# Optimization experiments

Hardware: AMD Instinct MI355X
Metric: run time of the kernel (lower is better)

Reference implementation:

```python
import math
import jax, jax.numpy as jnp
import numpy as np

B, S, D, H, F = 2, 2048, 1024, 16, 4096
HD = D // H
EPS = 1e-6
ALPHA, BETA = 0.5, 1.0  # SpectralActivation defaults


def setup_inputs() -> dict:
    key = jax.random.key(0)
    ks = jax.random.split(key, 24)
    init = lambda k, shape: (jax.random.normal(k, shape, jnp.float32) * 0.02)
    return {
        "x": jax.random.normal(ks[0], (B, S, D), jnp.float32),
        # attention params (W stored as [in, out], i.e. y = x @ W + b)
        "Wq": init(ks[1], (D, D)), "bq": jnp.zeros((D,), jnp.float32),
        "Wk": init(ks[2], (D, D)), "bk": jnp.zeros((D,), jnp.float32),
        "Wv": init(ks[3], (D, D)), "bv": jnp.zeros((D,), jnp.float32),
        "Wo": init(ks[4], (D, D)), "bo": jnp.zeros((D,), jnp.float32),
        "resonance": jnp.ones((H, 1, 1), jnp.float32),
        "phase": jnp.zeros((H, 1, 1), jnp.float32),
        # norm1
        "g1": jnp.ones((D,), jnp.float32), "b1": jnp.zeros((D,), jnp.float32),
        "s1": jnp.full((1,), 0.1, jnp.float32),
        # FFN
        "W1": init(ks[5], (D, F)), "bf1": jnp.zeros((F,), jnp.float32),
        "W2": init(ks[6], (F, D)), "bf2": jnp.zeros((D,), jnp.float32),
        # norm2
        "g2": jnp.ones((D,), jnp.float32), "b2": jnp.zeros((D,), jnp.float32),
        "s2": jnp.full((1,), 0.1, jnp.float32),
    }


def _harmonic_ln(x, gamma, beta, stab):
    mean = jnp.mean(x, axis=-1, keepdims=True)
    std = jnp.std(x, axis=-1, keepdims=True, ddof=1)  # torch std is unbiased
    std = std + stab * jnp.sin(std * math.pi)
    return gamma * ((x - mean) / (std + EPS)) + beta


def _spectral_act(x):
    c = math.sqrt(2.0 / math.pi)
    gelu_like = 0.5 * x * (1.0 + jnp.tanh(c * (x + 0.044715 * x ** 3)))
    return gelu_like + ALPHA * jnp.sin(BETA * x)


def _forward(x, Wq, bq, Wk, bk, Wv, bv, Wo, bo, resonance, phase,
             g1, b1, s1, W1, bf1, W2, bf2, g2, b2, s2):
    Bq, Sq, _ = x.shape
    q = (x @ Wq + bq).reshape(Bq, Sq, H, HD).transpose(0, 2, 1, 3)  # [B,H,S,hd]
    k = (x @ Wk + bk).reshape(Bq, Sq, H, HD).transpose(0, 2, 1, 3)
    v = (x @ Wv + bv).reshape(Bq, Sq, H, HD).transpose(0, 2, 1, 3)

    scores = jnp.einsum('bhqd,bhkd->bhqk', q, k) / math.sqrt(HD)  # [B,H,S,S]
    scores = scores + resonance[None] * jnp.sin(scores + phase[None])
    attn = jax.nn.softmax(scores, axis=-1)
    out = jnp.einsum('bhqk,bhkd->bhqd', attn, v)
    out = out.transpose(0, 2, 1, 3).reshape(Bq, Sq, D)
    attn_out = out @ Wo + bo

    x = _harmonic_ln(x + attn_out, g1, b1, s1)
    ff = _spectral_act(x @ W1 + bf1) @ W2 + bf2
    x = _harmonic_ln(x + ff, g2, b2, s2)
    return x


def reference(x, Wq, bq, Wk, bk, Wv, bv, Wo, bo, resonance, phase,
              g1, b1, s1, W1, bf1, W2, bf2, g2, b2, s2):
    return _forward(x, Wq, bq, Wk, bk, Wv, bv, Wo, bo, resonance, phase,
                    g1, b1, s1, W1, bf1, W2, bf2, g2, b2, s2)
```

## Files before the change

### kernel.cpp

```cpp
#include <hip/hip_runtime.h>
#include <cstdint>
#include <cstddef>


typedef float  f32x4  __attribute__((ext_vector_type(4)));
typedef __bf16 bf16x8 __attribute__((ext_vector_type(8)));
typedef unsigned short u16x8 __attribute__((ext_vector_type(8)));
typedef unsigned short u16x4 __attribute__((ext_vector_type(4)));

#define MFMA_BF16(a, b, c) __builtin_amdgcn_mfma_f32_16x16x32_bf16((a), (b), (c), 0, 0, 0)

static __device__ __forceinline__ unsigned short f32_to_bf16(float f) {
  unsigned int u = __float_as_uint(f);
  u += 0x7fffu + ((u >> 16) & 1u);
  return (unsigned short)(u >> 16);
}
static __device__ __forceinline__ float bf16_to_f32(unsigned short h) {
  return __uint_as_float(((unsigned int)h) << 16);
}
static __device__ __forceinline__ bf16x8 lds_frag(const unsigned short* base, int byte) {
  return __builtin_bit_cast(bf16x8, *(const u16x8*)((const char*)base + byte));
}
static __device__ __forceinline__ float spectral_act(float x) {
  const float c = 0.7978845608028654f;
  float g = 0.5f * x * (1.0f + tanhf(c * (x + 0.044715f * x * x * x)));
  return g + 0.5f * __sinf(x);
}

__global__ __launch_bounds__(256) void cvt_f32_bf16(const float* __restrict__ in,
                                                    unsigned short* __restrict__ out, int n) {
  int i = (blockIdx.x * 256 + threadIdx.x) * 4;
  if (i < n) {
    float4 v = *(const float4*)(in + i);
    u16x4 o;
    o[0] = f32_to_bf16(v.x); o[1] = f32_to_bf16(v.y);
    o[2] = f32_to_bf16(v.z); o[3] = f32_to_bf16(v.w);
    *(u16x4*)(out + i) = o;
  }
}

__global__ __launch_bounds__(256) void transpose_f32_bf16(const float* __restrict__ W,
                                                          unsigned short* __restrict__ Wt,
                                                          int K, int N) {
  __shared__ float tile[32][33];
  int tx = threadIdx.x & 31, ty = threadIdx.x >> 5;
  int k0 = blockIdx.y * 32, n0 = blockIdx.x * 32;
#pragma unroll
  for (int i = 0; i < 4; i++)
    tile[ty + i * 8][tx] = W[(size_t)(k0 + ty + i * 8) * N + n0 + tx];
  __syncthreads();
#pragma unroll
  for (int i = 0; i < 4; i++)
    Wt[(size_t)(n0 + ty + i * 8) * K + k0 + tx] = f32_to_bf16(tile[tx][ty + i * 8]);
}

template <int BM, int BN, int EPI>
__global__ __launch_bounds__(256) void gemm_bt(const unsigned short* __restrict__ A,
                                               const unsigned short* __restrict__ Bt,
                                               const float* __restrict__ bias,
                                               unsigned short* __restrict__ Cb,
                                               float* __restrict__ Cf,
                                               int M, int N, int K) {
  constexpr int MI = BM / 32;
  constexpr int NI = BN / 32;
  __shared__ unsigned short As[BM * 32];
  __shared__ unsigned short Bs[BN * 32];
  const int t = threadIdx.x;
  const int lane = t & 63, w = t >> 6;
  const int wr = w >> 1, wc = w & 1;
  const int g = lane >> 4, cc = lane & 15;
  const int row0 = blockIdx.y * BM, col0 = blockIdx.x * BN;

  f32x4 acc[MI][NI];
#pragma unroll
  for (int mi = 0; mi < MI; mi++)
#pragma unroll
    for (int ni = 0; ni < NI; ni++) acc[mi][ni] = (f32x4){0.f, 0.f, 0.f, 0.f};

  const int nk = K >> 5;
  const int sr = t >> 2, sc = (t & 3) * 8;

  for (int kt = 0; kt < nk; ++kt) {
    __syncthreads();
#pragma unroll
    for (int i = 0; i < BM / 64; ++i) {
      int r = sr + i * 64;
      u16x8 v = *(const u16x8*)(A + (size_t)(row0 + r) * K + (kt << 5) + sc);
      *(u16x8*)((char*)As + ((r * 64 + sc * 2) ^ ((r & 7) << 4))) = v;
    }
#pragma unroll
    for (int i = 0; i < BN / 64; ++i) {
      int r = sr + i * 64;
      u16x8 v = *(const u16x8*)(Bt + (size_t)(col0 + r) * K + (kt << 5) + sc);
      *(u16x8*)((char*)Bs + ((r * 64 + sc * 2) ^ ((r & 7) << 4))) = v;
    }
    __syncthreads();

    bf16x8 af[MI], bg[NI];
#pragma unroll
    for (int mi = 0; mi < MI; mi++) {
      int r = wr * (BM / 2) + mi * 16 + cc;
      af[mi] = lds_frag(As, (r * 64 + g * 16) ^ ((r & 7) << 4));
    }
#pragma unroll
    for (int ni = 0; ni < NI; ni++) {
      int r = wc * (BN / 2) + ni * 16 + cc;
      bg[ni] = lds_frag(Bs, (r * 64 + g * 16) ^ ((r & 7) << 4));
    }
#pragma unroll
    for (int mi = 0; mi < MI; mi++)
#pragma unroll
      for (int ni = 0; ni < NI; ni++)
        acc[mi][ni] = MFMA_BF16(af[mi], bg[ni], acc[mi][ni]);
  }

#pragma unroll
  for (int mi = 0; mi < MI; mi++) {
#pragma unroll
    for (int ni = 0; ni < NI; ni++) {
      int col = col0 + wc * (BN / 2) + ni * 16 + cc;
      float bv = bias[col];
#pragma unroll
      for (int r4 = 0; r4 < 4; r4++) {
        int row = row0 + wr * (BM / 2) + mi * 16 + g * 4 + r4;
        float val = acc[mi][ni][r4] + bv;
        if (EPI == 2) val = spectral_act(val);
        if (EPI == 0 || EPI == 2) Cb[(size_t)row * N + col] = f32_to_bf16(val);
        else                      Cf[(size_t)row * N + col] = val;
      }
    }
  }
}

__global__ __launch_bounds__(256) void attn_fused(const unsigned short* __restrict__ Qb,
                                                  const unsigned short* __restrict__ Kb,
                                                  const unsigned short* __restrict__ Vb,
                                                  int ld,
                                                  const float* __restrict__ resonance,
                                                  const float* __restrict__ phase,
                                                  unsigned short* __restrict__ O, int ldo) {
  constexpr int S = 2048;
  __shared__ unsigned short Ks[64 * 64];
  __shared__ unsigned short Vs[64 * 64];
  __shared__ unsigned short Ps[4][16 * 64];

  const int t = threadIdx.x, lane = t & 63, w = t >> 6;
  const int g = lane >> 4, cc = lane & 15;
  const int bh = blockIdx.y, b = bh >> 4, h = bh & 15;
  const int q0 = blockIdx.x * 64 + w * 16;
  const float res = resonance[h], ph = phase[h];

  const unsigned short* Qh = Qb + (size_t)b * S * ld + h * 64;
  const unsigned short* Kh = Kb + (size_t)b * S * ld + h * 64;
  const unsigned short* Vh = Vb + (size_t)b * S * ld + h * 64;

  bf16x8 qa0, qa1;
  {
    const unsigned short* qp = Qh + (size_t)(q0 + cc) * ld + g * 8;
    qa0 = __builtin_bit_cast(bf16x8, *(const u16x8*)qp);
    qa1 = __builtin_bit_cast(bf16x8, *(const u16x8*)(qp + 32));
  }

  f32x4 oacc[4];
#pragma unroll
  for (int i = 0; i < 4; i++) oacc[i] = (f32x4){0.f, 0.f, 0.f, 0.f};
  float Mx[4] = {-1e30f, -1e30f, -1e30f, -1e30f};
  float Lx[4] = {0.f, 0.f, 0.f, 0.f};
  char* PsW = (char*)&Ps[w][0];

  for (int kt = 0; kt < S / 64; ++kt) {
    __syncthreads();
    {
      int r = t >> 3, c8 = (t & 7) * 8;
      const unsigned short* kp = Kh + (size_t)(kt * 64) * ld;
#pragma unroll
      for (int hh = 0; hh < 2; ++hh) {
        int row = r + hh * 32;
        u16x8 v = *(const u16x8*)(kp + (size_t)row * ld + c8);
        *(u16x8*)((char*)Ks + ((row * 128 + c8 * 2) ^ ((row & 7) << 4))) = v;
      }
      int key = t & 63, hb0 = (t >> 6) * 16;
      const unsigned short* vp = Vh + (size_t)(kt * 64 + key) * ld + hb0;
      u16x8 v0 = *(const u16x8*)vp;
      u16x8 v1 = *(const u16x8*)(vp + 8);
#pragma unroll
      for (int j = 0; j < 8; j++) {
        int hd0 = hb0 + j;
        *(unsigned short*)((char*)Vs + ((hd0 * 128 + key * 2) ^ ((hd0 & 7) << 4))) = v0[j];
        int hd1 = hb0 + 8 + j;
        *(unsigned short*)((char*)Vs + ((hd1 * 128 + key * 2) ^ ((hd1 & 7) << 4))) = v1[j];
      }
    }
    __syncthreads();

    f32x4 sacc[4];
#pragma unroll
    for (int nb = 0; nb < 4; nb++) sacc[nb] = (f32x4){0.f, 0.f, 0.f, 0.f};
#pragma unroll
    for (int nb = 0; nb < 4; nb++) {
      int key = nb * 16 + cc;
      int rb = key * 128, xr = (key & 7) << 4;
      bf16x8 k0 = lds_frag(Ks, (rb + g * 16) ^ xr);
      bf16x8 k1 = lds_frag(Ks, (rb + 64 + g * 16) ^ xr);
      sacc[nb] = MFMA_BF16(qa0, k0, sacc[nb]);
      sacc[nb] = MFMA_BF16(qa1, k1, sacc[nb]);
    }

    float sm[4] = {-1e30f, -1e30f, -1e30f, -1e30f};
#pragma unroll
    for (int nb = 0; nb < 4; nb++)
#pragma unroll
      for (int r4 = 0; r4 < 4; r4++) {
        float sv = sacc[nb][r4] * 0.125f;
        sv += res * __sinf(sv + ph);
        sacc[nb][r4] = sv;
        sm[r4] = fmaxf(sm[r4], sv);
      }
#pragma unroll
    for (int d = 1; d < 16; d <<= 1)
#pragma unroll
      for (int r4 = 0; r4 < 4; r4++) sm[r4] = fmaxf(sm[r4], __shfl_xor(sm[r4], d, 16));

    float alpha[4], psum[4] = {0.f, 0.f, 0.f, 0.f};
#pragma unroll
    for (int r4 = 0; r4 < 4; r4++) {
      float nm = fmaxf(Mx[r4], sm[r4]);
      alpha[r4] = __expf(Mx[r4] - nm);
      Mx[r4] = nm;
    }
#pragma unroll
    for (int nb = 0; nb < 4; nb++)
#pragma unroll
      for (int r4 = 0; r4 < 4; r4++) {
        float p = __expf(sacc[nb][r4] - Mx[r4]);
        unsigned short pu = f32_to_bf16(p);
        psum[r4] += bf16_to_f32(pu);
        int prow = g * 4 + r4, pcol = nb * 16 + cc;
        *(unsigned short*)(PsW + ((prow * 128 + pcol * 2) ^ ((prow & 7) << 4))) = pu;
      }
#pragma unroll
    for (int d = 1; d < 16; d <<= 1)
#pragma unroll
      for (int r4 = 0; r4 < 4; r4++) psum[r4] += __shfl_xor(psum[r4], d, 16);
#pragma unroll
    for (int r4 = 0; r4 < 4; r4++) Lx[r4] = Lx[r4] * alpha[r4] + psum[r4];
#pragma unroll
    for (int nb2 = 0; nb2 < 4; nb2++)
#pragma unroll
      for (int r4 = 0; r4 < 4; r4++) oacc[nb2][r4] *= alpha[r4];

    bf16x8 pa0, pa1;
    {
      int xr = (cc & 7) << 4;
      pa0 = lds_frag((const unsigned short*)PsW, (cc * 128 + g * 16) ^ xr);
      pa1 = lds_frag((const unsigned short*)PsW, (cc * 128 + 64 + g * 16) ^ xr);
    }
#pragma unroll
    for (int nb2 = 0; nb2 < 4; nb2++) {
      int hd = nb2 * 16 + cc;
      int rb = hd * 128, xr = (hd & 7) << 4;
      bf16x8 v0 = lds_frag(Vs, (rb + g * 16) ^ xr);
      bf16x8 v1 = lds_frag(Vs, (rb + 64 + g * 16) ^ xr);
      oacc[nb2] = MFMA_BF16(pa0, v0, oacc[nb2]);
      oacc[nb2] = MFMA_BF16(pa1, v1, oacc[nb2]);
    }
  }

#pragma unroll
  for (int nb2 = 0; nb2 < 4; nb2++)
#pragma unroll
    for (int r4 = 0; r4 < 4; r4++) {
      float ov = oacc[nb2][r4] / Lx[r4];
      O[(size_t)(b * S + q0 + g * 4 + r4) * ldo + h * 64 + nb2 * 16 + cc] = f32_to_bf16(ov);
    }
}

__global__ __launch_bounds__(256) void resid_harmonic_ln(const float* __restrict__ xin,
                                                         const float* __restrict__ radd,
                                                         const float* __restrict__ gamma,
                                                         const float* __restrict__ beta,
                                                         const float* __restrict__ stab,
                                                         float* __restrict__ yf,
                                                         unsigned short* __restrict__ yb) {
  const int row = blockIdx.x, t = threadIdx.x;
  const float* xr = xin + (size_t)row * 1024;
  const float* rr = radd + (size_t)row * 1024;
  float v[4], s = 0.f, ss = 0.f;
#pragma unroll
  for (int j = 0; j < 4; j++) {
    int idx = t + j * 256;
    v[j] = xr[idx] + rr[idx];
    s += v[j]; ss += v[j] * v[j];
  }
#pragma unroll
  for (int d = 1; d < 64; d <<= 1) { s += __shfl_xor(s, d); ss += __shfl_xor(ss, d); }
  __shared__ float sb[8];
  int lane = t & 63, wid = t >> 6;
  if (lane == 0) { sb[wid] = s; sb[4 + wid] = ss; }
  __syncthreads();
  s = sb[0] + sb[1] + sb[2] + sb[3];
  ss = sb[4] + sb[5] + sb[6] + sb[7];
  float mean = s * (1.f / 1024.f);
  float var = fmaxf((ss - 1024.f * mean * mean) * (1.f / 1023.f), 0.f);
  float sd = sqrtf(var);
  sd += stab[0] * sinf(sd * 3.14159265358979323846f);
  float inv = 1.f / (sd + 1e-6f);
#pragma unroll
  for (int j = 0; j < 4; j++) {
    int idx = t + j * 256;
    float y = gamma[idx] * ((v[j] - mean) * inv) + beta[idx];
    yf[(size_t)row * 1024 + idx] = y;
    if (yb) yb[(size_t)row * 1024 + idx] = f32_to_bf16(y);
  }
}

extern "C" void kernel_launch(void* const* d_in, const int* in_sizes, int n_in,
                              void* d_out, int out_size, void* d_ws, size_t ws_size,
                              hipStream_t stream) {
  const float* x    = (const float*)d_in[0];
  const float* Wq   = (const float*)d_in[1];
  const float* bq   = (const float*)d_in[2];
  const float* Wk   = (const float*)d_in[3];
  const float* bk   = (const float*)d_in[4];
  const float* Wv   = (const float*)d_in[5];
  const float* bv   = (const float*)d_in[6];
  const float* Wo   = (const float*)d_in[7];
  const float* bo   = (const float*)d_in[8];
  const float* reso = (const float*)d_in[9];
  const float* phas = (const float*)d_in[10];
  const float* g1   = (const float*)d_in[11];
  const float* b1   = (const float*)d_in[12];
  const float* s1   = (const float*)d_in[13];
  const float* W1   = (const float*)d_in[14];
  const float* bf1  = (const float*)d_in[15];
  const float* W2   = (const float*)d_in[16];
  const float* bf2  = (const float*)d_in[17];
  const float* g2   = (const float*)d_in[18];
  const float* b2   = (const float*)d_in[19];
  const float* s2   = (const float*)d_in[20];

  const int BS = 4096;

  char* ws = (char*)d_ws;
  const size_t OFF_QKV  = 0;
  const size_t OFF_XB   = 25165824;
  const size_t OFF_WQKV = 33554432;
  const size_t OFF_WOT  = 39845888;
  const size_t OFF_W1T  = 41943040;
  const size_t OFF_W2T  = 50331648;
  const size_t OFF_BQKV = 58720256;
  const size_t OFF_T0   = 58736640;
  const size_t OFF_X1   = 75513856;
  const size_t OFF_X1B  = 92291072;

  unsigned short* qkv   = (unsigned short*)(ws + OFF_QKV);
  unsigned short* xb    = (unsigned short*)(ws + OFF_XB);
  unsigned short* ao    = (unsigned short*)(ws + OFF_XB);
  unsigned short* Wqkvt = (unsigned short*)(ws + OFF_WQKV);
  unsigned short* Wot   = (unsigned short*)(ws + OFF_WOT);
  unsigned short* W1t   = (unsigned short*)(ws + OFF_W1T);
  unsigned short* W2t   = (unsigned short*)(ws + OFF_W2T);
  float*          bqkv  = (float*)(ws + OFF_BQKV);
  float*          t0    = (float*)(ws + OFF_T0);
  float*          x1    = (float*)(ws + OFF_X1);
  unsigned short* x1b   = (unsigned short*)(ws + OFF_X1B);
  unsigned short* hb    = (unsigned short*)(ws + OFF_QKV);
  float*          out   = (float*)d_out;

  cvt_f32_bf16<<<4096, 256, 0, stream>>>(x, xb, BS * 1024);

  transpose_f32_bf16<<<dim3(32, 32), 256, 0, stream>>>(Wq, Wqkvt, 1024, 1024);
  transpose_f32_bf16<<<dim3(32, 32), 256, 0, stream>>>(Wk, Wqkvt + (size_t)1024 * 1024, 1024, 1024);
  transpose_f32_bf16<<<dim3(32, 32), 256, 0, stream>>>(Wv, Wqkvt + (size_t)2048 * 1024, 1024, 1024);
  transpose_f32_bf16<<<dim3(32, 32), 256, 0, stream>>>(Wo, Wot, 1024, 1024);
  transpose_f32_bf16<<<dim3(128, 32), 256, 0, stream>>>(W1, W1t, 1024, 4096);
  transpose_f32_bf16<<<dim3(32, 128), 256, 0, stream>>>(W2, W2t, 4096, 1024);

  hipMemcpyAsync((void*)bqkv,          (const void*)bq, 1024 * 4, hipMemcpyDeviceToDevice, stream);
  hipMemcpyAsync((void*)(bqkv + 1024), (const void*)bk, 1024 * 4, hipMemcpyDeviceToDevice, stream);
  hipMemcpyAsync((void*)(bqkv + 2048), (const void*)bv, 1024 * 4, hipMemcpyDeviceToDevice, stream);

  gemm_bt<128, 128, 0><<<dim3(24, 32), 256, 0, stream>>>(xb, Wqkvt, bqkv, qkv, nullptr,
                                                         4096, 3072, 1024);

  attn_fused<<<dim3(32, 32), 256, 0, stream>>>(qkv, qkv + 1024, qkv + 2048, 3072,
                                               reso, phas, ao, 1024);

  gemm_bt<128, 64, 1><<<dim3(16, 32), 256, 0, stream>>>(ao, Wot, bo, nullptr, t0,
                                                        4096, 1024, 1024);

  resid_harmonic_ln<<<4096, 256, 0, stream>>>(x, t0, g1, b1, s1, x1, x1b);

  gemm_bt<128, 128, 2><<<dim3(32, 32), 256, 0, stream>>>(x1b, W1t, bf1, hb, nullptr,
                                                         4096, 4096, 1024);

  gemm_bt<128, 64, 1><<<dim3(16, 32), 256, 0, stream>>>(hb, W2t, bf2, nullptr, t0,
                                                        4096, 1024, 4096);

  resid_harmonic_ln<<<4096, 256, 0, stream>>>(x1, t0, g2, b2, s2, out, nullptr);
}
```

Baseline: 528.9 us.

## Use direct global-to-LDS loads in GEMM and transposed LDS reads for V in attention

The GEMM tile loads now use global_load_lds to write straight into shared memory with a new XOR chunk swizzle, and the barrier moves to the end of each k iteration. In attention, V is stored row-major in per-block LDS tiles and read with ds_read_b64_tr_b16 transposed reads, replacing 16 scalar scattered LDS stores per thread. The softmax row sum is computed by an MFMA against a ones vector instead of shuffle reductions, and the bf16 conversion uses the hardware cast. These changes target LDS store traffic and VALU work, but depend on getting the swizzle and transposed-read address mapping exactly right.

```diff
diff --git a/kernel.cpp b/kernel.cpp
--- a/kernel.cpp
+++ b/kernel.cpp
@@ -7,16 +7,13 @@
 typedef __bf16 bf16x8 __attribute__((ext_vector_type(8)));
 typedef unsigned short u16x8 __attribute__((ext_vector_type(8)));
 typedef unsigned short u16x4 __attribute__((ext_vector_type(4)));
+typedef unsigned int   u32x2 __attribute__((ext_vector_type(2)));
+typedef unsigned int   u32x4 __attribute__((ext_vector_type(4)));
 
 #define MFMA_BF16(a, b, c) __builtin_amdgcn_mfma_f32_16x16x32_bf16((a), (b), (c), 0, 0, 0)
 
 static __device__ __forceinline__ unsigned short f32_to_bf16(float f) {
-  unsigned int u = __float_as_uint(f);
-  u += 0x7fffu + ((u >> 16) & 1u);
-  return (unsigned short)(u >> 16);
-}
-static __device__ __forceinline__ float bf16_to_f32(unsigned short h) {
-  return __uint_as_float(((unsigned int)h) << 16);
+  return __builtin_bit_cast(unsigned short, (__bf16)f);
 }
 static __device__ __forceinline__ bf16x8 lds_frag(const unsigned short* base, int byte) {
   return __builtin_bit_cast(bf16x8, *(const u16x8*)((const char*)base + byte));
@@ -25,6 +22,16 @@
   const float c = 0.7978845608028654f;
   float g = 0.5f * x * (1.0f + tanhf(c * (x + 0.044715f * x * x * x)));
   return g + 0.5f * __sinf(x);
+}
+static __device__ __forceinline__ void gload_lds16(const void* g, void* lds) {
+  __builtin_amdgcn_global_load_lds((const __attribute__((address_space(1))) unsigned int*)g,
+                                   (__attribute__((address_space(3))) unsigned int*)lds,
+                                   16, 0, 0);
+}
+static __device__ __forceinline__ u32x2 tr_read(unsigned addr) {
+  u32x2 r;
+  asm volatile("ds_read_b64_tr_b16 %0, %1" : "=v"(r) : "v"(addr));
+  return r;
 }
 
 __global__ __launch_bounds__(256) void cvt_f32_bf16(const float* __restrict__ in,
@@ -78,21 +85,21 @@
     for (int ni = 0; ni < NI; ni++) acc[mi][ni] = (f32x4){0.f, 0.f, 0.f, 0.f};
 
   const int nk = K >> 5;
-  const int sr = t >> 2, sc = (t & 3) * 8;
+  const int srow = lane >> 2;
+  const int schunk = (lane & 3) ^ ((lane >> 2) & 3);
 
   for (int kt = 0; kt < nk; ++kt) {
-    __syncthreads();
 #pragma unroll
     for (int i = 0; i < BM / 64; ++i) {
-      int r = sr + i * 64;
-      u16x8 v = *(const u16x8*)(A + (size_t)(row0 + r) * K + (kt << 5) + sc);
-      *(u16x8*)((char*)As + ((r * 64 + sc * 2) ^ ((r & 7) << 4))) = v;
+      int r = i * 64 + w * 16 + srow;
+      gload_lds16(A + (size_t)(row0 + r) * K + (kt << 5) + schunk * 8,
+                  As + (i * 64 + w * 16) * 32);
     }
 #pragma unroll
     for (int i = 0; i < BN / 64; ++i) {
-      int r = sr + i * 64;
-      u16x8 v = *(const u16x8*)(Bt + (size_t)(col0 + r) * K + (kt << 5) + sc);
-      *(u16x8*)((char*)Bs + ((r * 64 + sc * 2) ^ ((r & 7) << 4))) = v;
+      int r = i * 64 + w * 16 + srow;
+      gload_lds16(Bt + (size_t)(col0 + r) * K + (kt << 5) + schunk * 8,
+                  Bs + (i * 64 + w * 16) * 32);
     }
     __syncthreads();
 
@@ -100,18 +107,19 @@
 #pragma unroll
     for (int mi = 0; mi < MI; mi++) {
       int r = wr * (BM / 2) + mi * 16 + cc;
-      af[mi] = lds_frag(As, (r * 64 + g * 16) ^ ((r & 7) << 4));
+      af[mi] = lds_frag(As, r * 64 + ((g ^ (cc & 3)) << 4));
     }
 #pragma unroll
     for (int ni = 0; ni < NI; ni++) {
       int r = wc * (BN / 2) + ni * 16 + cc;
-      bg[ni] = lds_frag(Bs, (r * 64 + g * 16) ^ ((r & 7) << 4));
+      bg[ni] = lds_frag(Bs, r * 64 + ((g ^ (cc & 3)) << 4));
     }
 #pragma unroll
     for (int mi = 0; mi < MI; mi++)
 #pragma unroll
       for (int ni = 0; ni < NI; ni++)
         acc[mi][ni] = MFMA_BF16(af[mi], bg[ni], acc[mi][ni]);
+    __syncthreads();
   }
 
 #pragma unroll
@@ -141,7 +149,7 @@
                                                   unsigned short* __restrict__ O, int ldo) {
   constexpr int S = 2048;
   __shared__ unsigned short Ks[64 * 64];
-  __shared__ unsigned short Vs[64 * 64];
+  __shared__ unsigned short Vs[4][64 * 16];
   __shared__ unsigned short Ps[4][16 * 64];
 
   const int t = threadIdx.x, lane = t & 63, w = t >> 6;
@@ -161,6 +169,15 @@
     qa1 = __builtin_bit_cast(bf16x8, *(const u16x8*)(qp + 32));
   }
 
+  bf16x8 ones8;
+#pragma unroll
+  for (int j = 0; j < 8; j++) ones8[j] = (__bf16)1.0f;
+
+  const unsigned vs_base = (unsigned)(uintptr_t)(void*)&Vs[0][0];
+  const unsigned tr_a = vs_base + (unsigned)((8 * g + (cc >> 2)) * 32 +
+                                             (((cc & 2) >> 1) ^ (g & 1)) * 16 +
+                                             (cc & 1) * 8);
+
   f32x4 oacc[4];
 #pragma unroll
   for (int i = 0; i < 4; i++) oacc[i] = (f32x4){0.f, 0.f, 0.f, 0.f};
@@ -179,17 +196,14 @@
         u16x8 v = *(const u16x8*)(kp + (size_t)row * ld + c8);
         *(u16x8*)((char*)Ks + ((row * 128 + c8 * 2) ^ ((row & 7) << 4))) = v;
       }
-      int key = t & 63, hb0 = (t >> 6) * 16;
-      const unsigned short* vp = Vh + (size_t)(kt * 64 + key) * ld + hb0;
+      int key = t & 63, bb = t >> 6;
+      const unsigned short* vp = Vh + (size_t)(kt * 64 + key) * ld + bb * 16;
       u16x8 v0 = *(const u16x8*)vp;
       u16x8 v1 = *(const u16x8*)(vp + 8);
-#pragma unroll
-      for (int j = 0; j < 8; j++) {
-        int hd0 = hb0 + j;
-        *(unsigned short*)((char*)Vs + ((hd0 * 128 + key * 2) ^ ((hd0 & 7) << 4))) = v0[j];
-        int hd1 = hb0 + 8 + j;
-        *(unsigned short*)((char*)Vs + ((hd1 * 128 + key * 2) ^ ((hd1 & 7) << 4))) = v1[j];
-      }
+      int sw = (key >> 3) & 1;
+      char* vb = (char*)&Vs[bb][0] + key * 32;
+      *(u16x8*)(vb + sw * 16) = v0;
+      *(u16x8*)(vb + (1 - sw) * 16) = v1;
     }
     __syncthreads();
 
@@ -221,7 +235,7 @@
 #pragma unroll
       for (int r4 = 0; r4 < 4; r4++) sm[r4] = fmaxf(sm[r4], __shfl_xor(sm[r4], d, 16));
 
-    float alpha[4], psum[4] = {0.f, 0.f, 0.f, 0.f};
+    float alpha[4];
 #pragma unroll
     for (int r4 = 0; r4 < 4; r4++) {
       float nm = fmaxf(Mx[r4], sm[r4]);
@@ -233,21 +247,10 @@
 #pragma unroll
       for (int r4 = 0; r4 < 4; r4++) {
         float p = __expf(sacc[nb][r4] - Mx[r4]);
-        unsigned short pu = f32_to_bf16(p);
-        psum[r4] += bf16_to_f32(pu);
         int prow = g * 4 + r4, pcol = nb * 16 + cc;
-        *(unsigned short*)(PsW + ((prow * 128 + pcol * 2) ^ ((prow & 7) << 4))) = pu;
+        *(unsigned short*)(PsW + ((prow * 128 + pcol * 2) ^ ((prow & 7) << 4))) =
+            f32_to_bf16(p);
       }
-#pragma unroll
-    for (int d = 1; d < 16; d <<= 1)
-#pragma unroll
-      for (int r4 = 0; r4 < 4; r4++) psum[r4] += __shfl_xor(psum[r4], d, 16);
-#pragma unroll
-    for (int r4 = 0; r4 < 4; r4++) Lx[r4] = Lx[r4] * alpha[r4] + psum[r4];
-#pragma unroll
-    for (int nb2 = 0; nb2 < 4; nb2++)
-#pragma unroll
-      for (int r4 = 0; r4 < 4; r4++) oacc[nb2][r4] *= alpha[r4];
 
     bf16x8 pa0, pa1;
     {
@@ -255,14 +258,35 @@
       pa0 = lds_frag((const unsigned short*)PsW, (cc * 128 + g * 16) ^ xr);
       pa1 = lds_frag((const unsigned short*)PsW, (cc * 128 + 64 + g * 16) ^ xr);
     }
-#pragma unroll
-    for (int nb2 = 0; nb2 < 4; nb2++) {
-      int hd = nb2 * 16 + cc;
-      int rb = hd * 128, xr = (hd & 7) << 4;
-      bf16x8 v0 = lds_frag(Vs, (rb + g * 16) ^ xr);
-      bf16x8 v1 = lds_frag(Vs, (rb + 64 + g * 16) ^ xr);
-      oacc[nb2] = MFMA_BF16(pa0, v0, oacc[nb2]);
-      oacc[nb2] = MFMA_BF16(pa1, v1, oacc[nb2]);
+    f32x4 pacc = (f32x4){0.f, 0.f, 0.f, 0.f};
+    pacc = MFMA_BF16(pa0, ones8, pacc);
+    pacc = MFMA_BF16(pa1, ones8, pacc);
+#pragma unroll
+    for (int r4 = 0; r4 < 4; r4++) Lx[r4] = Lx[r4] * alpha[r4] + pacc[r4];
+#pragma unroll
+    for (int nb2 = 0; nb2 < 4; nb2++)
+#pragma unroll
+      for (int r4 = 0; r4 < 4; r4++) oacc[nb2][r4] *= alpha[r4];
+
+    u32x2 trv[4][4];
+#pragma unroll
+    for (int b2 = 0; b2 < 4; b2++) {
+      unsigned a = tr_a + b2 * 2048;
+      trv[b2][0] = tr_read(a);
+      trv[b2][1] = tr_read(a + 128);
+      trv[b2][2] = tr_read(a + 1024);
+      trv[b2][3] = tr_read(a + 1152);
+    }
+    asm volatile("s_waitcnt lgkmcnt(0)" ::: "memory");
+    __builtin_amdgcn_sched_barrier(0);
+#pragma unroll
+    for (int b2 = 0; b2 < 4; b2++) {
+      bf16x8 v0 = __builtin_bit_cast(bf16x8,
+          (u32x4){trv[b2][0][0], trv[b2][0][1], trv[b2][1][0], trv[b2][1][1]});
+      bf16x8 v1 = __builtin_bit_cast(bf16x8,
+          (u32x4){trv[b2][2][0], trv[b2][2][1], trv[b2][3][0], trv[b2][3][1]});
+      oacc[b2] = MFMA_BF16(pa0, v0, oacc[b2]);
+      oacc[b2] = MFMA_BF16(pa1, v1, oacc[b2]);
     }
   }
 
```

Result: no change. 524.7 us (-0.8%).
